# Performance work log

Hardware: AMD Instinct MI355X
Metric: run time of the kernel (lower is better)

Reference implementation:

```python
import jax, jax.numpy as jnp
import numpy as np

N = 50000      # nodes
E = 600000     # edges
F_IN = 128
F_OUT = 128
R = 4          # num_relations
BN_EPS = 1e-5  # PyTorch BatchNorm1d default


def setup_inputs() -> dict:
    key = jax.random.key(0)
    ks = jax.random.split(key, 8)
    s = 1.0 / np.sqrt(F_IN)
    return {
        "x": jax.random.normal(ks[0], (N, F_IN), jnp.float32),
        "edge_index": jax.random.randint(ks[1], (2, E), 0, N),
        "edge_type": jax.random.randint(ks[2], (E,), 0, R),
        "W_self": jax.random.uniform(ks[3], (F_IN, F_OUT), jnp.float32, -s, s),
        "b_self": jnp.zeros((F_OUT,), jnp.float32),
        "W1": jax.random.uniform(ks[4], (R, F_IN, F_OUT), jnp.float32, -s, s),
        "b1": jnp.zeros((R, F_OUT), jnp.float32),
        "gamma": jnp.ones((R, F_OUT), jnp.float32),
        "beta": jnp.zeros((R, F_OUT), jnp.float32),
        "W2": jax.random.uniform(ks[5], (R, F_OUT, F_OUT), jnp.float32, -s, s),
        "b2": jnp.zeros((R, F_OUT), jnp.float32),
    }


def reference(x, edge_index, edge_type, W_self, b_self, W1, b1, gamma, beta, W2, b2):
    row, col = edge_index[0], edge_index[1]
    # Per-relation scatter-add aggregation in one segment_sum pass:
    # segment id = relation * N + destination row.
    seg = edge_type * N + row
    agg = jax.ops.segment_sum(x[col], seg, num_segments=R * N)
    agg = agg.reshape(R, N, F_IN)
    # GIN update with eps=0: h_r = x + agg_r
    h = x[None, :, :] + agg                              # (R, N, F_IN)
    # Per-relation MLP: Linear -> BatchNorm(train stats) -> ReLU -> Linear
    h = jnp.einsum('rnf,rfo->rno', h, W1) + b1[:, None, :]
    mean = jnp.mean(h, axis=1, keepdims=True)
    var = jnp.var(h, axis=1, keepdims=True)              # biased, as in BN
    h = (h - mean) * jax.lax.rsqrt(var + BN_EPS)
    h = h * gamma[:, None, :] + beta[:, None, :]
    h = jax.nn.relu(h)
    h = jnp.einsum('rno,rop->rnp', h, W2) + b2[:, None, :]
    # Self-loop linear plus sum over relations
    return x @ W_self + b_self + jnp.sum(h, axis=0)
```

## Files before the change

### kernel.cpp

```cpp
#include <hip/hip_runtime.h>

#define Nn 50000
#define Ee 600000
#define Rr 4
#define NBIN 200704
#define BN_EPS 1e-5f
#define ECAP 2048

typedef __bf16 bfrag  __attribute__((ext_vector_type(8)));
typedef float  f32x4  __attribute__((ext_vector_type(4)));

__device__ __forceinline__ unsigned short f2b(float f) {
    union { float f; unsigned int u; } v; v.f = f;
    return (unsigned short)((v.u + 0x7FFFu + ((v.u >> 16) & 1u)) >> 16);
}
__device__ __forceinline__ float b2f(unsigned short u) {
    union { unsigned int u; float f; } v; v.u = ((unsigned int)u) << 16; return v.f;
}

__global__ __launch_bounds__(256) void prep_k(
    const float* __restrict__ x, const float* __restrict__ W1,
    const float* __restrict__ W2, const float* __restrict__ Wself,
    const int* __restrict__ ei, const int* __restrict__ et,
    unsigned int* __restrict__ xb, unsigned short* __restrict__ WT,
    int* __restrict__ hist)
{
    int b = blockIdx.x;
    if (b < 12500) {
        int i = b * 256 + threadIdx.x;
        float2 v = ((const float2*)x)[i];
        xb[i] = ((unsigned int)f2b(v.y) << 16) | f2b(v.x);
    } else if (b < 13076) {
        int idx = (b - 12500) * 256 + threadIdx.x;
        int mat = idx >> 14, rem = idx & 16383;
        int n = rem >> 7, k = rem & 127;
        const float* src = (mat < 4) ? (W1 + mat * 16384)
                         : (mat < 8) ? (W2 + (mat - 4) * 16384) : Wself;
        WT[idx] = f2b(src[k * 128 + n]);
    } else {
        int e = (b - 13076) * 256 + threadIdx.x;
        if (e < Ee) atomicAdd(&hist[et[e] * Nn + ei[e]], 1);
    }
}

__global__ __launch_bounds__(256) void scan1_k(
    const int* __restrict__ hist, int* __restrict__ offs, int* __restrict__ bsum)
{
    int t = threadIdx.x, b = blockIdx.x;
    int base = b * 1024 + t * 4;
    int4 c = *(const int4*)(hist + base);
    int s = c.x + c.y + c.z + c.w;
    __shared__ int tmp[256];
    tmp[t] = s; __syncthreads();
    for (int off = 1; off < 256; off <<= 1) {
        int v = (t >= off) ? tmp[t - off] : 0;
        __syncthreads(); tmp[t] += v; __syncthreads();
    }
    int excl = tmp[t] - s;
    int4 o; o.x = excl; o.y = excl + c.x; o.z = o.y + c.y; o.w = o.z + c.z;
    *(int4*)(offs + base) = o;
    if (t == 255) bsum[b] = tmp[255];
}
__global__ __launch_bounds__(256) void scan3_k(
    int* __restrict__ offs, int* __restrict__ cur, const int* __restrict__ bsum)
{
    int t = threadIdx.x, b = blockIdx.x;
    __shared__ int tmp[256];
    tmp[t] = (t < b) ? bsum[t] : 0;
    __syncthreads();
    for (int off = 128; off > 0; off >>= 1) {
        if (t < off) tmp[t] += tmp[t + off];
        __syncthreads();
    }
    int add = tmp[0];
    int base = b * 1024 + t * 4;
    int4 o = *(int4*)(offs + base);
    o.x += add; o.y += add; o.z += add; o.w += add;
    *(int4*)(offs + base) = o;
    *(int4*)(cur + base) = o;
}

__global__ __launch_bounds__(256) void fill_k(
    const int* __restrict__ ei, const int* __restrict__ et,
    int* __restrict__ cur, int* __restrict__ ssrc)
{
    int e = blockIdx.x * 256 + threadIdx.x;
    if (e >= Ee) return;
    int bin = et[e] * Nn + ei[e];
    int pos = atomicAdd(&cur[bin], 1);
    ssrc[pos] = ei[Ee + e];
}

#define ACC_QUAD(u0_, u1_, u2_, u3_)                                      \
    do {                                                                  \
        unsigned int uu[16] = {u0_.x,u0_.y,u0_.z,u0_.w, u1_.x,u1_.y,u1_.z,u1_.w, \
                               u2_.x,u2_.y,u2_.z,u2_.w, u3_.x,u3_.y,u3_.z,u3_.w}; \
        _Pragma("unroll")                                                 \
        for (int jj = 0; jj < 16; ++jj) {                                 \
            acc[2*jj]   += b2f((unsigned short)(uu[jj] & 0xFFFF));        \
            acc[2*jj+1] += b2f((unsigned short)(uu[jj] >> 16));           \
        }                                                                 \
    } while (0)

__global__ __launch_bounds__(512) void gemm1f_k(
    const unsigned int* __restrict__ xb, const int* __restrict__ offs,
    const int* __restrict__ ssrc, const unsigned short* __restrict__ WT,
    const float* __restrict__ b1, unsigned short* __restrict__ h,
    float* __restrict__ gsum, float* __restrict__ gsq)
{
    const int r  = blockIdx.y;
    const int n0 = blockIdx.x * 128;
    const int t  = threadIdx.x;

    __shared__ __attribute__((aligned(16))) __bf16 As[128][136];
    __shared__ __attribute__((aligned(16))) __bf16 Ws[128][136];
    __shared__ float s_sum[128], s_sq[128];
    __shared__ int s_off[129];
    __shared__ int s_edge[ECAP];

    if (t < 128) { s_sum[t] = 0.f; s_sq[t] = 0.f; }
    const int rows = (Nn - n0 < 128) ? (Nn - n0) : 128;
    if (t <= rows) s_off[t] = offs[r * Nn + n0 + t];
    __syncthreads();

    const int ebeg = s_off[0];
    const int ecnt = s_off[rows] - ebeg;
    const bool inl = (ecnt <= ECAP);
    if (inl) for (int i = t; i < ecnt; i += 512) s_edge[i] = ssrc[ebeg + i];
    {
        const unsigned short* Wr = WT + r * 16384;
        for (int i = t; i < 2048; i += 512) {
            int n = i >> 4, kc = (i & 15) << 3;
            *(uint4*)&Ws[n][kc] = *(const uint4*)(Wr + n * 128 + kc);
        }
    }
    __syncthreads();

    {
        const int row = t >> 2, q = t & 3, gm = n0 + row;
        float acc[32];
#pragma unroll
        for (int j = 0; j < 32; ++j) acc[j] = 0.f;
        if (gm < Nn) {
            const uint4* xr = (const uint4*)(xb + (size_t)gm * 64 + q * 16);
            uint4 u0 = xr[0], u1 = xr[1], u2 = xr[2], u3 = xr[3];
            ACC_QUAD(u0, u1, u2, u3);
            int jb = s_off[row] - ebeg, je = s_off[row + 1] - ebeg;
            if (jb < je) {
                int s0 = inl ? s_edge[jb] : ssrc[ebeg + jb];
                const uint4* p = (const uint4*)(xb + (size_t)s0 * 64 + q * 16);
                uint4 c0 = p[0], c1 = p[1], c2 = p[2], c3 = p[3];
                for (int j = jb + 1; ; ++j) {
                    uint4 d0, d1, d2, d3;
                    const bool more = (j < je);
                    if (more) {
                        int s1 = inl ? s_edge[j] : ssrc[ebeg + j];
                        const uint4* pn = (const uint4*)(xb + (size_t)s1 * 64 + q * 16);
                        d0 = pn[0]; d1 = pn[1]; d2 = pn[2]; d3 = pn[3];
                    }
                    ACC_QUAD(c0, c1, c2, c3);
                    if (!more) break;
                    c0 = d0; c1 = d1; c2 = d2; c3 = d3;
                }
            }
        }
        unsigned int pk[16];
#pragma unroll
        for (int j = 0; j < 16; ++j)
            pk[j] = ((unsigned int)f2b(acc[2*j+1]) << 16) | f2b(acc[2*j]);
        uint4* dst = (uint4*)&As[row][q * 32];
        dst[0] = make_uint4(pk[0],  pk[1],  pk[2],  pk[3]);
        dst[1] = make_uint4(pk[4],  pk[5],  pk[6],  pk[7]);
        dst[2] = make_uint4(pk[8],  pk[9],  pk[10], pk[11]);
        dst[3] = make_uint4(pk[12], pk[13], pk[14], pk[15]);
    }
    __syncthreads();

    const int w = t >> 6, l = t & 63, ln = l & 15, quad = l >> 4;
    f32x4 acc2[8];
#pragma unroll
    for (int c = 0; c < 8; ++c) acc2[c] = (f32x4){0.f,0.f,0.f,0.f};
#pragma unroll
    for (int kk = 0; kk < 4; ++kk) {
        int ks = kk * 32 + quad * 8;
        bfrag a = *(const bfrag*)&As[w * 16 + ln][ks];
#pragma unroll
        for (int c = 0; c < 8; ++c) {
            bfrag b = *(const bfrag*)&Ws[c * 16 + ln][ks];
            acc2[c] = __builtin_amdgcn_mfma_f32_16x16x32_bf16(a, b, acc2[c], 0, 0, 0);
        }
    }
    __syncthreads();

#pragma unroll
    for (int c = 0; c < 8; ++c) {
        int col = c * 16 + ln;
        float bias = b1[r * 128 + col];
        float ps = 0.f, pq = 0.f;
#pragma unroll
        for (int reg = 0; reg < 4; ++reg) {
            int lrow = w * 16 + quad * 4 + reg;
            float v = acc2[c][reg] + bias;
            As[lrow][col] = (__bf16)v;
            if (n0 + lrow < Nn) { ps += v; pq += v * v; }
        }
        ps += __shfl_xor(ps, 16); pq += __shfl_xor(pq, 16);
        ps += __shfl_xor(ps, 32); pq += __shfl_xor(pq, 32);
        if (quad == 0) { atomicAdd(&s_sum[col], ps); atomicAdd(&s_sq[col], pq); }
    }
    __syncthreads();

    unsigned short* hr = h + (size_t)r * Nn * 128;
    for (int i = t; i < 2048; i += 512) {
        int m = i >> 4, kc = (i & 15) << 3;
        int gm = n0 + m;
        if (gm < Nn) *(uint4*)(hr + (size_t)gm * 128 + kc) = *(const uint4*)&As[m][kc];
    }
    if (t < 128) {
        atomicAdd(&gsum[r * 128 + t], s_sum[t]);
        atomicAdd(&gsq[r * 128 + t],  s_sq[t]);
    }
}

__global__ void finalize_k(
    const float* __restrict__ gsum, const float* __restrict__ gsq,
    const float* __restrict__ gamma, const float* __restrict__ beta,
    float* __restrict__ coefA, float* __restrict__ coefC)
{
    int i = threadIdx.x;
    float mean = gsum[i] * (1.0f / Nn);
    float var  = gsq[i] * (1.0f / Nn) - mean * mean;
    float a    = gamma[i] * rsqrtf(fmaxf(var, 0.f) + BN_EPS);
    coefA[i] = a;
    coefC[i] = beta[i] - mean * a;
}

__global__ __launch_bounds__(512) void gemm2f_k(
    const unsigned int* __restrict__ xb,
    const unsigned short* __restrict__ h,
    const unsigned short* __restrict__ WT,
    const float* __restrict__ bself, const float* __restrict__ b2,
    const float* __restrict__ coefA, const float* __restrict__ coefC,
    float* __restrict__ out)
{
    const int n0 = blockIdx.x * 128;
    const int t  = threadIdx.x;
    __shared__ __attribute__((aligned(16))) __bf16 As[128][136];
    __shared__ __attribute__((aligned(16))) __bf16 Ws[128][136];

    const int w = t >> 6, l = t & 63, ln = l & 15, quad = l >> 4;
    f32x4 acc2[8];
#pragma unroll
    for (int c = 0; c < 8; ++c) acc2[c] = (f32x4){0.f,0.f,0.f,0.f};

    for (int rr = 0; rr < 5; ++rr) {
        const unsigned short* Wr = WT + (rr < 4 ? (4 + rr) : 8) * 16384;
        for (int i = t; i < 2048; i += 512) {
            int n = i >> 4, kc = (i & 15) << 3;
            *(uint4*)&Ws[n][kc] = *(const uint4*)(Wr + n * 128 + kc);
        }
        if (rr < 4) {
            const unsigned short* hrp = h + (size_t)rr * Nn * 128;
            const float* cA = coefA + rr * 128;
            const float* cC = coefC + rr * 128;
            for (int i = t; i < 2048; i += 512) {
                int m = i >> 4, kc = (i & 15) << 3;
                int gm = n0 + m;
                uint4 hv = make_uint4(0,0,0,0);
                if (gm < Nn) hv = *(const uint4*)(hrp + (size_t)gm * 128 + kc);
                unsigned int hu[4] = {hv.x, hv.y, hv.z, hv.w};
                unsigned int pk[4];
#pragma unroll
                for (int j = 0; j < 4; ++j) {
                    float v0 = fmaxf(cA[kc + 2*j]     * b2f((unsigned short)(hu[j] & 0xFFFF)) + cC[kc + 2*j],     0.f);
                    float v1 = fmaxf(cA[kc + 2*j + 1] * b2f((unsigned short)(hu[j] >> 16))    + cC[kc + 2*j + 1], 0.f);
                    pk[j] = ((unsigned int)f2b(v1) << 16) | f2b(v0);
                }
                *(uint4*)&As[m][kc] = make_uint4(pk[0], pk[1], pk[2], pk[3]);
            }
        } else {
            for (int i = t; i < 2048; i += 512) {
                int m = i >> 4, kc = (i & 15) << 3;
                int gm = n0 + m;
                uint4 v = make_uint4(0, 0, 0, 0);
                if (gm < Nn) v = *(const uint4*)(xb + (size_t)gm * 64 + (kc >> 1));
                *(uint4*)&As[m][kc] = v;
            }
        }
        __syncthreads();
#pragma unroll
        for (int kk = 0; kk < 4; ++kk) {
            int ks = kk * 32 + quad * 8;
            bfrag a = *(const bfrag*)&As[w * 16 + ln][ks];
#pragma unroll
            for (int c = 0; c < 8; ++c) {
                bfrag b = *(const bfrag*)&Ws[c * 16 + ln][ks];
                acc2[c] = __builtin_amdgcn_mfma_f32_16x16x32_bf16(a, b, acc2[c], 0, 0, 0);
            }
        }
        __syncthreads();
    }

    float bias[8];
#pragma unroll
    for (int c = 0; c < 8; ++c) {
        int col = c * 16 + ln;
        bias[c] = bself[col] + b2[col] + b2[128 + col] + b2[256 + col] + b2[384 + col];
    }
    float* fws = (float*)Ws;
    for (int p = 0; p < 2; ++p) {
        if ((w >> 2) == p) {
#pragma unroll
            for (int c = 0; c < 8; ++c) {
                int lrow = (w & 3) * 16 + quad * 4;
                int col  = c * 16 + ln;
#pragma unroll
                for (int reg = 0; reg < 4; ++reg)
                    fws[(lrow + reg) * 132 + col] = acc2[c][reg] + bias[c];
            }
        }
        __syncthreads();
        for (int i = t; i < 2048; i += 512) {
            int m = i >> 5, kc = (i & 31) << 2;
            int gm = n0 + p * 64 + m;
            if (gm < Nn)
                *(float4*)(out + (size_t)gm * 128 + kc) = *(const float4*)&fws[m * 132 + kc];
        }
        __syncthreads();
    }
}

extern "C" void kernel_launch(void* const* d_in, const int* in_sizes, int n_in,
                              void* d_out, int out_size, void* d_ws, size_t ws_size,
                              hipStream_t stream) {
    const float* x     = (const float*)d_in[0];
    const int*   ei    = (const int*)d_in[1];
    const int*   et    = (const int*)d_in[2];
    const float* Wself = (const float*)d_in[3];
    const float* bself = (const float*)d_in[4];
    const float* W1    = (const float*)d_in[5];
    const float* b1    = (const float*)d_in[6];
    const float* gamma = (const float*)d_in[7];
    const float* beta  = (const float*)d_in[8];
    const float* W2    = (const float*)d_in[9];
    const float* b2    = (const float*)d_in[10];
    float* out = (float*)d_out;

    char* ws = (char*)d_ws;
    int*   hist  = (int*)(ws + 0);
    float* gsum  = (float*)(ws + 802816);
    float* gsq   = (float*)(ws + 804864);
    float* coefA = (float*)(ws + 806912);
    float* coefC = (float*)(ws + 808960);
    int*   bsum  = (int*)(ws + 811008);
    int*   offs  = (int*)(ws + 813056);
    int*   cur   = (int*)(ws + 1615872);
    int*   ssrc  = (int*)(ws + 2418688);
    unsigned short* h  = (unsigned short*)(ws + 4818688);
    unsigned int*   xb = (unsigned int*)(ws + 56018688);
    unsigned short* WT = (unsigned short*)(ws + 68818688);

    (void)hipMemsetAsync(ws, 0, 806912, stream);

    const int EB = (Ee + 255) / 256;
    prep_k <<<12500 + 576 + EB, 256, 0, stream>>>(x, W1, W2, Wself, ei, et, xb, WT, hist);
    scan1_k<<<196, 256, 0, stream>>>(hist, offs, bsum);
    scan3_k<<<196, 256, 0, stream>>>(offs, cur, bsum);
    fill_k <<<EB, 256, 0, stream>>>(ei, et, cur, ssrc);

    dim3 g1((Nn + 127) / 128, Rr);
    gemm1f_k<<<g1, 512, 0, stream>>>(xb, offs, ssrc, WT, b1, h, gsum, gsq);
    finalize_k<<<1, 512, 0, stream>>>(gsum, gsq, gamma, beta, coefA, coefC);
    gemm2f_k<<<(Nn + 127) / 128, 512, 0, stream>>>(
        xb, h, WT, bself, b2, coefA, coefC, out);
}
```

Measured before the change: 269.4 us.

## Process two relations per gemm1 block and fold BN finalize into gemm2

```diff
diff --git a/kernel.cpp b/kernel.cpp
--- a/kernel.cpp
+++ b/kernel.cpp
@@ -5,7 +5,7 @@
 #define Rr 4
 #define NBIN 200704
 #define BN_EPS 1e-5f
-#define ECAP 2048
+#define ECAP 1024
 
 typedef __bf16 bfrag  __attribute__((ext_vector_type(8)));
 typedef float  f32x4  __attribute__((ext_vector_type(4)));
@@ -91,14 +91,14 @@
     ssrc[pos] = ei[Ee + e];
 }
 
-#define ACC_QUAD(u0_, u1_, u2_, u3_)                                      \
+#define ACC_QUADP(A_, u0_, u1_, u2_, u3_)                                 \
     do {                                                                  \
         unsigned int uu[16] = {u0_.x,u0_.y,u0_.z,u0_.w, u1_.x,u1_.y,u1_.z,u1_.w, \
                                u2_.x,u2_.y,u2_.z,u2_.w, u3_.x,u3_.y,u3_.z,u3_.w}; \
         _Pragma("unroll")                                                 \
         for (int jj = 0; jj < 16; ++jj) {                                 \
-            acc[2*jj]   += b2f((unsigned short)(uu[jj] & 0xFFFF));        \
-            acc[2*jj+1] += b2f((unsigned short)(uu[jj] >> 16));           \
+            A_[2*jj]   += b2f((unsigned short)(uu[jj] & 0xFFFF));         \
+            A_[2*jj+1] += b2f((unsigned short)(uu[jj] >> 16));            \
         }                                                                 \
     } while (0)
 
@@ -108,27 +108,29 @@
     const float* __restrict__ b1, unsigned short* __restrict__ h,
     float* __restrict__ gsum, float* __restrict__ gsq)
 {
-    const int r  = blockIdx.y;
+    const int r0 = blockIdx.y * 2, r1 = r0 + 1;
     const int n0 = blockIdx.x * 128;
     const int t  = threadIdx.x;
 
     __shared__ __attribute__((aligned(16))) __bf16 As[128][136];
     __shared__ __attribute__((aligned(16))) __bf16 Ws[128][136];
-    __shared__ float s_sum[128], s_sq[128];
-    __shared__ int s_off[129];
-    __shared__ int s_edge[ECAP];
-
-    if (t < 128) { s_sum[t] = 0.f; s_sq[t] = 0.f; }
+    __shared__ float s_sum[256], s_sq[256];
+    __shared__ int s_off0[129], s_off1[129];
+    __shared__ int s_e0[ECAP], s_e1[ECAP];
+
+    if (t < 256) { s_sum[t] = 0.f; s_sq[t] = 0.f; }
     const int rows = (Nn - n0 < 128) ? (Nn - n0) : 128;
-    if (t <= rows) s_off[t] = offs[r * Nn + n0 + t];
-    __syncthreads();
-
-    const int ebeg = s_off[0];
-    const int ecnt = s_off[rows] - ebeg;
-    const bool inl = (ecnt <= ECAP);
-    if (inl) for (int i = t; i < ecnt; i += 512) s_edge[i] = ssrc[ebeg + i];
+    if (t <= rows) s_off0[t] = offs[r0 * Nn + n0 + t];
+    else if (t >= 256 && t - 256 <= rows) s_off1[t - 256] = offs[r1 * Nn + n0 + (t - 256)];
+    __syncthreads();
+
+    const int eb0 = s_off0[0], ec0 = s_off0[rows] - eb0;
+    const int eb1 = s_off1[0], ec1 = s_off1[rows] - eb1;
+    const bool inl0 = (ec0 <= ECAP), inl1 = (ec1 <= ECAP);
+    if (inl0) for (int i = t; i < ec0; i += 512) s_e0[i] = ssrc[eb0 + i];
+    if (inl1) for (int i = t; i < ec1; i += 512) s_e1[i] = ssrc[eb1 + i];
     {
-        const unsigned short* Wr = WT + r * 16384;
+        const unsigned short* Wr = WT + r0 * 16384;
         for (int i = t; i < 2048; i += 512) {
             int n = i >> 4, kc = (i & 15) << 3;
             *(uint4*)&Ws[n][kc] = *(const uint4*)(Wr + n * 128 + kc);
@@ -136,50 +138,55 @@
     }
     __syncthreads();
 
+    unsigned int pk1[16];
     {
         const int row = t >> 2, q = t & 3, gm = n0 + row;
-        float acc[32];
-#pragma unroll
-        for (int j = 0; j < 32; ++j) acc[j] = 0.f;
+        float a0[32], a1[32];
+#pragma unroll
+        for (int j = 0; j < 32; ++j) { a0[j] = 0.f; a1[j] = 0.f; }
         if (gm < Nn) {
             const uint4* xr = (const uint4*)(xb + (size_t)gm * 64 + q * 16);
             uint4 u0 = xr[0], u1 = xr[1], u2 = xr[2], u3 = xr[3];
-            ACC_QUAD(u0, u1, u2, u3);
-            int jb = s_off[row] - ebeg, je = s_off[row + 1] - ebeg;
-            if (jb < je) {
-                int s0 = inl ? s_edge[jb] : ssrc[ebeg + jb];
-                const uint4* p = (const uint4*)(xb + (size_t)s0 * 64 + q * 16);
-                uint4 c0 = p[0], c1 = p[1], c2 = p[2], c3 = p[3];
-                for (int j = jb + 1; ; ++j) {
-                    uint4 d0, d1, d2, d3;
-                    const bool more = (j < je);
-                    if (more) {
-                        int s1 = inl ? s_edge[j] : ssrc[ebeg + j];
-                        const uint4* pn = (const uint4*)(xb + (size_t)s1 * 64 + q * 16);
-                        d0 = pn[0]; d1 = pn[1]; d2 = pn[2]; d3 = pn[3];
-                    }
-                    ACC_QUAD(c0, c1, c2, c3);
-                    if (!more) break;
-                    c0 = d0; c1 = d1; c2 = d2; c3 = d3;
+            ACC_QUADP(a0, u0, u1, u2, u3);
+#pragma unroll
+            for (int j = 0; j < 32; ++j) a1[j] = a0[j];
+            int j0 = s_off0[row] - eb0, je0 = s_off0[row + 1] - eb0;
+            int j1 = s_off1[row] - eb1, je1 = s_off1[row + 1] - eb1;
+            while (j0 < je0 || j1 < je1) {
+                bool m0 = j0 < je0, m1 = j1 < je1;
+                uint4 c0, c1, c2, c3, e0, e1, e2, e3;
+                if (m0) {
+                    int s = inl0 ? s_e0[j0] : ssrc[eb0 + j0];
+                    const uint4* p = (const uint4*)(xb + (size_t)s * 64 + q * 16);
+                    c0 = p[0]; c1 = p[1]; c2 = p[2]; c3 = p[3];
                 }
+                if (m1) {
+                    int s = inl1 ? s_e1[j1] : ssrc[eb1 + j1];
+                    const uint4* p = (const uint4*)(xb + (size_t)s * 64 + q * 16);
+                    e0 = p[0]; e1 = p[1]; e2 = p[2]; e3 = p[3];
+                }
+                if (m0) { ACC_QUADP(a0, c0, c1, c2, c3); ++j0; }
+                if (m1) { ACC_QUADP(a1, e0, e1, e2, e3); ++j1; }
             }
         }
-        unsigned int pk[16];
-#pragma unroll
-        for (int j = 0; j < 16; ++j)
-            pk[j] = ((unsigned int)f2b(acc[2*j+1]) << 16) | f2b(acc[2*j]);
+        unsigned int pk0[16];
+#pragma unroll
+        for (int j = 0; j < 16; ++j) {
+            pk0[j] = ((unsigned int)f2b(a0[2*j+1]) << 16) | f2b(a0[2*j]);
+            pk1[j] = ((unsigned int)f2b(a1[2*j+1]) << 16) | f2b(a1[2*j]);
+        }
         uint4* dst = (uint4*)&As[row][q * 32];
-        dst[0] = make_uint4(pk[0],  pk[1],  pk[2],  pk[3]);
-        dst[1] = make_uint4(pk[4],  pk[5],  pk[6],  pk[7]);
-        dst[2] = make_uint4(pk[8],  pk[9],  pk[10], pk[11]);
-        dst[3] = make_uint4(pk[12], pk[13], pk[14], pk[15]);
+        dst[0] = make_uint4(pk0[0],  pk0[1],  pk0[2],  pk0[3]);
+        dst[1] = make_uint4(pk0[4],  pk0[5],  pk0[6],  pk0[7]);
+        dst[2] = make_uint4(pk0[8],  pk0[9],  pk0[10], pk0[11]);
+        dst[3] = make_uint4(pk0[12], pk0[13], pk0[14], pk0[15]);
     }
     __syncthreads();
 
     const int w = t >> 6, l = t & 63, ln = l & 15, quad = l >> 4;
-    f32x4 acc2[8];
-#pragma unroll
-    for (int c = 0; c < 8; ++c) acc2[c] = (f32x4){0.f,0.f,0.f,0.f};
+    f32x4 acc0[8];
+#pragma unroll
+    for (int c = 0; c < 8; ++c) acc0[c] = (f32x4){0.f,0.f,0.f,0.f};
 #pragma unroll
     for (int kk = 0; kk < 4; ++kk) {
         int ks = kk * 32 + quad * 8;
@@ -187,52 +194,85 @@
 #pragma unroll
         for (int c = 0; c < 8; ++c) {
             bfrag b = *(const bfrag*)&Ws[c * 16 + ln][ks];
-            acc2[c] = __builtin_amdgcn_mfma_f32_16x16x32_bf16(a, b, acc2[c], 0, 0, 0);
-        }
-    }
-    __syncthreads();
-
+            acc0[c] = __builtin_amdgcn_mfma_f32_16x16x32_bf16(a, b, acc0[c], 0, 0, 0);
+        }
+    }
+    __syncthreads();
+
+    {
+        const int row = t >> 2, q = t & 3;
+        uint4* dst = (uint4*)&As[row][q * 32];
+        dst[0] = make_uint4(pk1[0],  pk1[1],  pk1[2],  pk1[3]);
+        dst[1] = make_uint4(pk1[4],  pk1[5],  pk1[6],  pk1[7]);
+        dst[2] = make_uint4(pk1[8],  pk1[9],  pk1[10], pk1[11]);
+        dst[3] = make_uint4(pk1[12], pk1[13], pk1[14], pk1[15]);
+        const unsigned short* Wr = WT + r1 * 16384;
+        for (int i = t; i < 2048; i += 512) {
+            int n = i >> 4, kc = (i & 15) << 3;
+            *(uint4*)&Ws[n][kc] = *(const uint4*)(Wr + n * 128 + kc);
+        }
+    }
+    __syncthreads();
+
+    f32x4 acc1[8];
+#pragma unroll
+    for (int c = 0; c < 8; ++c) acc1[c] = (f32x4){0.f,0.f,0.f,0.f};
+#pragma unroll
+    for (int kk = 0; kk < 4; ++kk) {
+        int ks = kk * 32 + quad * 8;
+        bfrag a = *(const bfrag*)&As[w * 16 + ln][ks];
+#pragma unroll
+        for (int c = 0; c < 8; ++c) {
+            bfrag b = *(const bfrag*)&Ws[c * 16 + ln][ks];
+            acc1[c] = __builtin_amdgcn_mfma_f32_16x16x32_bf16(a, b, acc1[c], 0, 0, 0);
+        }
+    }
+    __syncthreads();
+
+    __bf16 (*Hs)[136] = (__bf16(*)[136])Ws;
 #pragma unroll
     for (int c = 0; c < 8; ++c) {
         int col = c * 16 + ln;
-        float bias = b1[r * 128 + col];
-        float ps = 0.f, pq = 0.f;
+        float bias0 = b1[r0 * 128 + col];
+        float bias1 = b1[r1 * 128 + col];
+        float ps0 = 0.f, pq0 = 0.f, ps1 = 0.f, pq1 = 0.f;
 #pragma unroll
         for (int reg = 0; reg < 4; ++reg) {
             int lrow = w * 16 + quad * 4 + reg;
-            float v = acc2[c][reg] + bias;
-            As[lrow][col] = (__bf16)v;
-            if (n0 + lrow < Nn) { ps += v; pq += v * v; }
-        }
-        ps += __shfl_xor(ps, 16); pq += __shfl_xor(pq, 16);
-        ps += __shfl_xor(ps, 32); pq += __shfl_xor(pq, 32);
-        if (quad == 0) { atomicAdd(&s_sum[col], ps); atomicAdd(&s_sq[col], pq); }
-    }
-    __syncthreads();
-
-    unsigned short* hr = h + (size_t)r * Nn * 128;
+            float v0 = acc0[c][reg] + bias0;
+            float v1 = acc1[c][reg] + bias1;
+            As[lrow][col] = (__bf16)v0;
+            Hs[lrow][col] = (__bf16)v1;
+            if (n0 + lrow < Nn) { ps0 += v0; pq0 += v0 * v0; ps1 += v1; pq1 += v1 * v1; }
+        }
+        ps0 += __shfl_xor(ps0, 16); pq0 += __shfl_xor(pq0, 16);
+        ps0 += __shfl_xor(ps0, 32); pq0 += __shfl_xor(pq0, 32);
+        ps1 += __shfl_xor(ps1, 16); pq1 += __shfl_xor(pq1, 16);
+        ps1 += __shfl_xor(ps1, 32); pq1 += __shfl_xor(pq1, 32);
+        if (quad == 0) {
+            atomicAdd(&s_sum[col], ps0);       atomicAdd(&s_sq[col], pq0);
+            atomicAdd(&s_sum[128 + col], ps1); atomicAdd(&s_sq[128 + col], pq1);
+        }
+    }
+    __syncthreads();
+
+    unsigned short* hr0 = h + (size_t)r0 * Nn * 128;
+    unsigned short* hr1 = h + (size_t)r1 * Nn * 128;
     for (int i = t; i < 2048; i += 512) {
         int m = i >> 4, kc = (i & 15) << 3;
         int gm = n0 + m;
-        if (gm < Nn) *(uint4*)(hr + (size_t)gm * 128 + kc) = *(const uint4*)&As[m][kc];
+        if (gm < Nn) {
+            *(uint4*)(hr0 + (size_t)gm * 128 + kc) = *(const uint4*)&As[m][kc];
+            *(uint4*)(hr1 + (size_t)gm * 128 + kc) = *(const uint4*)&Hs[m][kc];
+        }
     }
     if (t < 128) {
-        atomicAdd(&gsum[r * 128 + t], s_sum[t]);
-        atomicAdd(&gsq[r * 128 + t],  s_sq[t]);
-    }
-}
-
-__global__ void finalize_k(
-    const float* __restrict__ gsum, const float* __restrict__ gsq,
-    const float* __restrict__ gamma, const float* __restrict__ beta,
-    float* __restrict__ coefA, float* __restrict__ coefC)
-{
-    int i = threadIdx.x;
-    float mean = gsum[i] * (1.0f / Nn);
-    float var  = gsq[i] * (1.0f / Nn) - mean * mean;
-    float a    = gamma[i] * rsqrtf(fmaxf(var, 0.f) + BN_EPS);
-    coefA[i] = a;
-    coefC[i] = beta[i] - mean * a;
+        atomicAdd(&gsum[r0 * 128 + t], s_sum[t]);
+        atomicAdd(&gsq[r0 * 128 + t],  s_sq[t]);
+    } else if (t < 256) {
+        atomicAdd(&gsum[r1 * 128 + (t - 128)], s_sum[t]);
+        atomicAdd(&gsq[r1 * 128 + (t - 128)],  s_sq[t]);
+    }
 }
 
 __global__ __launch_bounds__(512) void gemm2f_k(
@@ -240,13 +280,24 @@
     const unsigned short* __restrict__ h,
     const unsigned short* __restrict__ WT,
     const float* __restrict__ bself, const float* __restrict__ b2,
-    const float* __restrict__ coefA, const float* __restrict__ coefC,
+    const float* __restrict__ gsum, const float* __restrict__ gsq,
+    const float* __restrict__ gamma, const float* __restrict__ beta,
     float* __restrict__ out)
 {
     const int n0 = blockIdx.x * 128;
     const int t  = threadIdx.x;
     __shared__ __attribute__((aligned(16))) __bf16 As[128][136];
     __shared__ __attribute__((aligned(16))) __bf16 Ws[128][136];
+    __shared__ float s_cA[512], s_cC[512];
+
+    {
+        float mean = gsum[t] * (1.0f / Nn);
+        float var  = gsq[t] * (1.0f / Nn) - mean * mean;
+        float a    = gamma[t] * rsqrtf(fmaxf(var, 0.f) + BN_EPS);
+        s_cA[t] = a;
+        s_cC[t] = beta[t] - mean * a;
+    }
+    __syncthreads();
 
     const int w = t >> 6, l = t & 63, ln = l & 15, quad = l >> 4;
     f32x4 acc2[8];
@@ -261,8 +312,8 @@
         }
         if (rr < 4) {
             const unsigned short* hrp = h + (size_t)rr * Nn * 128;
-            const float* cA = coefA + rr * 128;
-            const float* cC = coefC + rr * 128;
+            const float* cA = s_cA + rr * 128;
+            const float* cC = s_cC + rr * 128;
             for (int i = t; i < 2048; i += 512) {
                 int m = i >> 4, kc = (i & 15) << 3;
                 int gm = n0 + m;
@@ -350,8 +401,6 @@
     int*   hist  = (int*)(ws + 0);
     float* gsum  = (float*)(ws + 802816);
     float* gsq   = (float*)(ws + 804864);
-    float* coefA = (float*)(ws + 806912);
-    float* coefC = (float*)(ws + 808960);
     int*   bsum  = (int*)(ws + 811008);
     int*   offs  = (int*)(ws + 813056);
     int*   cur   = (int*)(ws + 1615872);
@@ -368,9 +417,8 @@
     scan3_k<<<196, 256, 0, stream>>>(offs, cur, bsum);
     fill_k <<<EB, 256, 0, stream>>>(ei, et, cur, ssrc);
 
-    dim3 g1((Nn + 127) / 128, Rr);
+    dim3 g1((Nn + 127) / 128, 2);
     gemm1f_k<<<g1, 512, 0, stream>>>(xb, offs, ssrc, WT, b1, h, gsum, gsq);
-    finalize_k<<<1, 512, 0, stream>>>(gsum, gsq, gamma, beta, coefA, coefC);
     gemm2f_k<<<(Nn + 127) / 128, 512, 0, stream>>>(
-        xb, h, WT, bself, b2, coefA, coefC, out);
-}
+        xb, h, WT, bself, b2, gsum, gsq, gamma, beta, out);
+}
```

Result: slower. 296.6 us (+10.1%).
